# Performance work log

Measured on AMD Instinct MI355X. Metric: run time of the kernel, lower is better.

## Reference

```python
import jax, jax.numpy as jnp
import numpy as np

B = 2_000_000
OVERLAP_WEIGHT = 0.5
EPS = 1e-6


def setup_inputs() -> dict:
    key = jax.random.key(0)
    k1, k2 = jax.random.split(key)
    preds = jax.random.normal(k1, (B, 10), dtype=jnp.float32)
    targets = jax.random.normal(k2, (B, 10), dtype=jnp.float32)
    return {"preds": preds, "targets": targets}


def _quat_to_rot(q):
    # q: (B,4) in xyzw order, assumed normalized. Returns (B,3,3),
    # matching the (transposed-convention) matrix in the torch source.
    x, y, z, w = q[:, 0], q[:, 1], q[:, 2], q[:, 3]
    r = jnp.stack([
        1 - 2 * y * y - 2 * z * z, 2 * x * y + 2 * z * w, 2 * x * z - 2 * y * w,
        2 * x * y - 2 * z * w, 1 - 2 * x * x - 2 * z * z, 2 * y * z + 2 * x * w,
        2 * x * z + 2 * y * w, 2 * y * z - 2 * x * w, 1 - 2 * x * x - 2 * y * y,
    ], axis=-1)
    return r.reshape(-1, 3, 3)


def _overlaps(pred_params, gt_params):
    pred_c, pred_d, pred_q = pred_params[:, :3], pred_params[:, 3:6], pred_params[:, 6:]
    gt_c, gt_d, gt_q = gt_params[:, :3], gt_params[:, 3:6], gt_params[:, 6:]
    pred_q = pred_q / jnp.linalg.norm(pred_q, axis=-1, keepdims=True)
    gt_q = gt_q / jnp.linalg.norm(gt_q, axis=-1, keepdims=True)
    pred_rot = _quat_to_rot(pred_q)  # (B,3,3)
    gt_rot = _quat_to_rot(gt_q)      # (B,3,3)
    # trace(pred_rot.T @ gt_rot) = sum of elementwise products
    rot_align = jnp.clip(jnp.sum(pred_rot * gt_rot, axis=(1, 2)) / 3.0, 0.0, 1.0)
    pred_ext = jnp.abs(jnp.einsum('bij,bj->bi', pred_rot, pred_d / 2))
    gt_ext = jnp.abs(jnp.einsum('bij,bj->bi', gt_rot, gt_d / 2))
    center_diff = jnp.abs(pred_c - gt_c)
    overlap_per_axis = jnp.maximum(jnp.minimum(pred_ext, gt_ext) * 2 - center_diff, 0.0) \
        / (pred_ext + gt_ext + EPS)
    overlap = jnp.prod(overlap_per_axis, axis=-1) * rot_align
    return jnp.clip(overlap, 0.0, 1.0)


def _smooth_l1(preds, targets):
    d = preds - targets
    ad = jnp.abs(d)
    return jnp.mean(jnp.where(ad < 1.0, 0.5 * d * d, ad - 0.5))


def reference(preds, targets):
    param_loss = _smooth_l1(preds, targets)
    overlap = _overlaps(preds, targets)
    return param_loss + OVERLAP_WEIGHT * (1.0 - jnp.mean(overlap))
```

## Files before the change

kernel.cpp:

```cpp
#include <hip/hip_runtime.h>


#define B_ROWS 2000000
#define THREADS 256
#define CHUNK_ROWS 512
#define CHUNK_F4 1280
#define N_CHUNKS 3907
#define GRID 1024
constexpr float OVERLAP_WEIGHT = 0.5f;
constexpr float EPS_F = 1e-6f;
constexpr int TOTAL_F4 = 5000000;

__device__ __forceinline__ void quat_to_rot(float x, float y, float z, float w,
                                            float R[9]) {
    R[0] = 1.f - 2.f*y*y - 2.f*z*z;
    R[1] = 2.f*x*y + 2.f*z*w;
    R[2] = 2.f*x*z - 2.f*y*w;
    R[3] = 2.f*x*y - 2.f*z*w;
    R[4] = 1.f - 2.f*x*x - 2.f*z*z;
    R[5] = 2.f*y*z + 2.f*x*w;
    R[6] = 2.f*x*z + 2.f*y*w;
    R[7] = 2.f*y*z - 2.f*x*w;
    R[8] = 1.f - 2.f*x*x - 2.f*y*y;
}

__global__ __launch_bounds__(THREADS) void hybrid_loss_main(
    const float4* __restrict__ preds4, const float4* __restrict__ targets4,
    float* __restrict__ acc)
{
    __shared__ __align__(16) float4 ldsP[CHUNK_F4];
    __shared__ __align__(16) float4 ldsT[CHUNK_F4];

    const int tid  = threadIdx.x;
    const int wave = tid >> 6;
    const int lane = tid & 63;
    const int spos = wave * 320 + lane;

    float4 rp[5], rt[5];
    float psum = 0.f, osum = 0.f;

    int c = blockIdx.x;
    {
        const int gb = c * CHUNK_F4;
        #pragma unroll
        for (int i = 0; i < 5; ++i) {
            int idx = gb + spos + i * 64;
            if (idx >= TOTAL_F4) idx = TOTAL_F4 - 1;
            rp[i] = preds4[idx];
            rt[i] = targets4[idx];
        }
    }

    while (true) {
        #pragma unroll
        for (int i = 0; i < 5; ++i) {
            ldsP[spos + i * 64] = rp[i];
            ldsT[spos + i * 64] = rt[i];
        }
        __syncthreads();

        const int cn = c + GRID;
        const bool more = (cn < N_CHUNKS);
        if (more) {
            const int gb = cn * CHUNK_F4;
            #pragma unroll
            for (int i = 0; i < 5; ++i) {
                int idx = gb + spos + i * 64;
                if (idx >= TOTAL_F4) idx = TOTAL_F4 - 1;
                rp[i] = preds4[idx];
                rt[i] = targets4[idx];
            }
        }

        const int rowbase = c * CHUNK_ROWS;
        #pragma unroll
        for (int k = 0; k < 2; ++k) {
            const int rr = tid + k * 256;
            if (rowbase + rr < B_ROWS) {
                float p[10], t[10];
                const float2* lp = reinterpret_cast<const float2*>(
                    reinterpret_cast<const float*>(ldsP) + rr * 10);
                const float2* lt = reinterpret_cast<const float2*>(
                    reinterpret_cast<const float*>(ldsT) + rr * 10);
                #pragma unroll
                for (int i = 0; i < 5; ++i) {
                    float2 a = lp[i]; p[2*i] = a.x; p[2*i+1] = a.y;
                    float2 b = lt[i]; t[2*i] = b.x; t[2*i+1] = b.y;
                }

                #pragma unroll
                for (int i = 0; i < 10; ++i) {
                    float d  = p[i] - t[i];
                    float ad = fabsf(d);
                    psum += (ad < 1.f) ? 0.5f * d * d : ad - 0.5f;
                }

                float pqn = sqrtf(p[6]*p[6] + p[7]*p[7] + p[8]*p[8] + p[9]*p[9]);
                float tqn = sqrtf(t[6]*t[6] + t[7]*t[7] + t[8]*t[8] + t[9]*t[9]);
                float pri = 1.f / pqn, tri = 1.f / tqn;
                float PR[9], TR[9];
                quat_to_rot(p[6]*pri, p[7]*pri, p[8]*pri, p[9]*pri, PR);
                quat_to_rot(t[6]*tri, t[7]*tri, t[8]*tri, t[9]*tri, TR);

                float ra = 0.f;
                #pragma unroll
                for (int i = 0; i < 9; ++i) ra += PR[i] * TR[i];
                ra = fminf(fmaxf(ra * (1.f/3.f), 0.f), 1.f);

                float ov = ra;
                #pragma unroll
                for (int i = 0; i < 3; ++i) {
                    float pe = fabsf(PR[3*i+0]*(p[3]*0.5f) + PR[3*i+1]*(p[4]*0.5f) + PR[3*i+2]*(p[5]*0.5f));
                    float te = fabsf(TR[3*i+0]*(t[3]*0.5f) + TR[3*i+1]*(t[4]*0.5f) + TR[3*i+2]*(t[5]*0.5f));
                    float cd = fabsf(p[i] - t[i]);
                    float ax = fmaxf(fminf(pe, te) * 2.f - cd, 0.f) / (pe + te + EPS_F);
                    ov *= ax;
                }
                ov = fminf(fmaxf(ov, 0.f), 1.f);
                osum += ov;
            }
        }
        __syncthreads();
        if (!more) break;
        c = cn;
    }

    #pragma unroll
    for (int off = 32; off > 0; off >>= 1) {
        psum += __shfl_down(psum, off);
        osum += __shfl_down(osum, off);
    }
    float* red = reinterpret_cast<float*>(ldsP);
    if (lane == 0) { red[wave] = psum; red[4 + wave] = osum; }
    __syncthreads();
    if (tid == 0) {
        float P = red[0] + red[1] + red[2] + red[3];
        float O = red[4] + red[5] + red[6] + red[7];
        atomicAdd(&acc[0], P);
        atomicAdd(&acc[1], O);
    }
}

__global__ void hybrid_loss_finalize(const float* __restrict__ acc,
                                     float* __restrict__ out) {
    out[0] = acc[0] * (1.f / (10.f * (float)B_ROWS))
           + OVERLAP_WEIGHT * (1.f - acc[1] * (1.f / (float)B_ROWS));
}

extern "C" void kernel_launch(void* const* d_in, const int* in_sizes, int n_in,
                              void* d_out, int out_size, void* d_ws, size_t ws_size,
                              hipStream_t stream) {
    const float4* preds4   = (const float4*)d_in[0];
    const float4* targets4 = (const float4*)d_in[1];
    float* out = (float*)d_out;
    float* acc = (float*)d_ws;

    hipMemsetAsync(acc, 0, 2 * sizeof(float), stream);

    hybrid_loss_main<<<GRID, THREADS, 0, stream>>>(preds4, targets4, acc);
    hybrid_loss_finalize<<<1, 1, 0, stream>>>(acc, out);
}
```

Baseline: 210.9 us.

## Stage tiles with direct global-to-LDS loads into double-buffered shared memory

```diff
diff --git a/kernel.cpp b/kernel.cpp
--- a/kernel.cpp
+++ b/kernel.cpp
@@ -3,13 +3,19 @@
 
 #define B_ROWS 2000000
 #define THREADS 256
-#define CHUNK_ROWS 512
-#define CHUNK_F4 1280
-#define N_CHUNKS 3907
+#define CHUNK_ROWS 256
+#define F4_SIDE 640
+#define N_CHUNKS 7813
 #define GRID 1024
 constexpr float OVERLAP_WEIGHT = 0.5f;
 constexpr float EPS_F = 1e-6f;
 constexpr int TOTAL_F4 = 5000000;
+
+__device__ __forceinline__ void gload_lds16(const float4* g, float4* l) {
+    __builtin_amdgcn_global_load_lds(
+        (const __attribute__((address_space(1))) void*)g,
+        (__attribute__((address_space(3))) void*)l, 16, 0, 0);
+}
 
 __device__ __forceinline__ void quat_to_rot(float x, float y, float z, float w,
                                             float R[9]) {
@@ -28,101 +34,82 @@
     const float4* __restrict__ preds4, const float4* __restrict__ targets4,
     float* __restrict__ acc)
 {
-    __shared__ __align__(16) float4 ldsP[CHUNK_F4];
-    __shared__ __align__(16) float4 ldsT[CHUNK_F4];
+    __shared__ __align__(16) float4 lds[2][2][F4_SIDE];
 
     const int tid  = threadIdx.x;
     const int wave = tid >> 6;
     const int lane = tid & 63;
-    const int spos = wave * 320 + lane;
 
-    float4 rp[5], rt[5];
     float psum = 0.f, osum = 0.f;
 
+    auto stage = [&](int buf, int c) {
+        const int gb = c * F4_SIDE;
+        for (int r = wave; r < 10; r += 4) {
+            int idx = gb + r * 64 + lane;
+            if (idx >= TOTAL_F4) idx = TOTAL_F4 - 1;
+            gload_lds16(preds4   + idx, &lds[buf][0][r * 64]);
+            gload_lds16(targets4 + idx, &lds[buf][1][r * 64]);
+        }
+    };
+
     int c = blockIdx.x;
-    {
-        const int gb = c * CHUNK_F4;
-        #pragma unroll
-        for (int i = 0; i < 5; ++i) {
-            int idx = gb + spos + i * 64;
-            if (idx >= TOTAL_F4) idx = TOTAL_F4 - 1;
-            rp[i] = preds4[idx];
-            rt[i] = targets4[idx];
-        }
-    }
+    int cur = 0;
+    stage(0, c);
+    __syncthreads();
 
     while (true) {
-        #pragma unroll
-        for (int i = 0; i < 5; ++i) {
-            ldsP[spos + i * 64] = rp[i];
-            ldsT[spos + i * 64] = rt[i];
-        }
-        __syncthreads();
-
         const int cn = c + GRID;
         const bool more = (cn < N_CHUNKS);
-        if (more) {
-            const int gb = cn * CHUNK_F4;
+        if (more) stage(cur ^ 1, cn);
+
+        if (c * CHUNK_ROWS + tid < B_ROWS) {
+            float p[10], t[10];
+            const float2* lp = reinterpret_cast<const float2*>(
+                reinterpret_cast<const float*>(&lds[cur][0][0]) + tid * 10);
+            const float2* lt = reinterpret_cast<const float2*>(
+                reinterpret_cast<const float*>(&lds[cur][1][0]) + tid * 10);
             #pragma unroll
             for (int i = 0; i < 5; ++i) {
-                int idx = gb + spos + i * 64;
-                if (idx >= TOTAL_F4) idx = TOTAL_F4 - 1;
-                rp[i] = preds4[idx];
-                rt[i] = targets4[idx];
+                float2 a = lp[i]; p[2*i] = a.x; p[2*i+1] = a.y;
+                float2 b = lt[i]; t[2*i] = b.x; t[2*i+1] = b.y;
             }
+
+            #pragma unroll
+            for (int i = 0; i < 10; ++i) {
+                float d  = p[i] - t[i];
+                float ad = fabsf(d);
+                psum += (ad < 1.f) ? 0.5f * d * d : ad - 0.5f;
+            }
+
+            float pqn = sqrtf(p[6]*p[6] + p[7]*p[7] + p[8]*p[8] + p[9]*p[9]);
+            float tqn = sqrtf(t[6]*t[6] + t[7]*t[7] + t[8]*t[8] + t[9]*t[9]);
+            float pri = 1.f / pqn, tri = 1.f / tqn;
+            float PR[9], TR[9];
+            quat_to_rot(p[6]*pri, p[7]*pri, p[8]*pri, p[9]*pri, PR);
+            quat_to_rot(t[6]*tri, t[7]*tri, t[8]*tri, t[9]*tri, TR);
+
+            float ra = 0.f;
+            #pragma unroll
+            for (int i = 0; i < 9; ++i) ra += PR[i] * TR[i];
+            ra = fminf(fmaxf(ra * (1.f/3.f), 0.f), 1.f);
+
+            float ov = ra;
+            #pragma unroll
+            for (int i = 0; i < 3; ++i) {
+                float pe = fabsf(PR[3*i+0]*(p[3]*0.5f) + PR[3*i+1]*(p[4]*0.5f) + PR[3*i+2]*(p[5]*0.5f));
+                float te = fabsf(TR[3*i+0]*(t[3]*0.5f) + TR[3*i+1]*(t[4]*0.5f) + TR[3*i+2]*(t[5]*0.5f));
+                float cd = fabsf(p[i] - t[i]);
+                float ax = fmaxf(fminf(pe, te) * 2.f - cd, 0.f) / (pe + te + EPS_F);
+                ov *= ax;
+            }
+            ov = fminf(fmaxf(ov, 0.f), 1.f);
+            osum += ov;
         }
 
-        const int rowbase = c * CHUNK_ROWS;
-        #pragma unroll
-        for (int k = 0; k < 2; ++k) {
-            const int rr = tid + k * 256;
-            if (rowbase + rr < B_ROWS) {
-                float p[10], t[10];
-                const float2* lp = reinterpret_cast<const float2*>(
-                    reinterpret_cast<const float*>(ldsP) + rr * 10);
-                const float2* lt = reinterpret_cast<const float2*>(
-                    reinterpret_cast<const float*>(ldsT) + rr * 10);
-                #pragma unroll
-                for (int i = 0; i < 5; ++i) {
-                    float2 a = lp[i]; p[2*i] = a.x; p[2*i+1] = a.y;
-                    float2 b = lt[i]; t[2*i] = b.x; t[2*i+1] = b.y;
-                }
-
-                #pragma unroll
-                for (int i = 0; i < 10; ++i) {
-                    float d  = p[i] - t[i];
-                    float ad = fabsf(d);
-                    psum += (ad < 1.f) ? 0.5f * d * d : ad - 0.5f;
-                }
-
-                float pqn = sqrtf(p[6]*p[6] + p[7]*p[7] + p[8]*p[8] + p[9]*p[9]);
-                float tqn = sqrtf(t[6]*t[6] + t[7]*t[7] + t[8]*t[8] + t[9]*t[9]);
-                float pri = 1.f / pqn, tri = 1.f / tqn;
-                float PR[9], TR[9];
-                quat_to_rot(p[6]*pri, p[7]*pri, p[8]*pri, p[9]*pri, PR);
-                quat_to_rot(t[6]*tri, t[7]*tri, t[8]*tri, t[9]*tri, TR);
-
-                float ra = 0.f;
-                #pragma unroll
-                for (int i = 0; i < 9; ++i) ra += PR[i] * TR[i];
-                ra = fminf(fmaxf(ra * (1.f/3.f), 0.f), 1.f);
-
-                float ov = ra;
-                #pragma unroll
-                for (int i = 0; i < 3; ++i) {
-                    float pe = fabsf(PR[3*i+0]*(p[3]*0.5f) + PR[3*i+1]*(p[4]*0.5f) + PR[3*i+2]*(p[5]*0.5f));
-                    float te = fabsf(TR[3*i+0]*(t[3]*0.5f) + TR[3*i+1]*(t[4]*0.5f) + TR[3*i+2]*(t[5]*0.5f));
-                    float cd = fabsf(p[i] - t[i]);
-                    float ax = fmaxf(fminf(pe, te) * 2.f - cd, 0.f) / (pe + te + EPS_F);
-                    ov *= ax;
-                }
-                ov = fminf(fmaxf(ov, 0.f), 1.f);
-                osum += ov;
-            }
-        }
         __syncthreads();
         if (!more) break;
         c = cn;
+        cur ^= 1;
     }
 
     #pragma unroll
@@ -130,7 +117,7 @@
         psum += __shfl_down(psum, off);
         osum += __shfl_down(osum, off);
     }
-    float* red = reinterpret_cast<float*>(ldsP);
+    float* red = reinterpret_cast<float*>(&lds[0][0][0]);
     if (lane == 0) { red[wave] = psum; red[4 + wave] = osum; }
     __syncthreads();
     if (tid == 0) {
```

New measurement: 191.2 us. -9.3%, faster.
